# Kernel optimization log

Measured on AMD Instinct MI355X. Metric: run time of the kernel, lower is better.

## Reference

```python
import jax, jax.numpy as jnp
import numpy as np
import math

SEQ_LEN = 1024
NUM_FILTERS = 24
INPUT_DIM = 256
OUTPUT_DIM = 256
BATCH = 4


def _spectral_filters(seq_len, K):
    # Hankel matrix Z[i,j] = 2 / ((i+j)^3 - (i+j)), i,j in 1..L (use_hankel_L=False)
    entries = np.arange(1, seq_len + 1, dtype=np.float64)
    ipj = entries[:, None] + entries[None, :]
    Z = 2.0 / (ipj ** 3 - ipj)
    sigma, phi = np.linalg.eigh(Z)
    phi_k = phi[:, -K:] * (sigma[-K:] ** 0.25)
    return jnp.asarray(phi_k, dtype=jnp.float32)  # [L, K]


def setup_inputs() -> dict:
    key = jax.random.key(0)
    k1, k2, k3 = jax.random.split(key, 3)
    scale = (NUM_FILTERS * INPUT_DIM) ** (-0.5)
    x = jax.random.normal(k1, (BATCH, SEQ_LEN, INPUT_DIM), dtype=jnp.float32)
    phi = _spectral_filters(SEQ_LEN, NUM_FILTERS)
    M_phi_plus = jax.random.normal(k2, (NUM_FILTERS, INPUT_DIM, OUTPUT_DIM), dtype=jnp.float32) * scale
    M_phi_minus = jax.random.normal(k3, (NUM_FILTERS, INPUT_DIM, OUTPUT_DIM), dtype=jnp.float32) * scale
    return {"x": x, "phi": phi, "M_phi_plus": M_phi_plus, "M_phi_minus": M_phi_minus}


def reference(x, phi, M_phi_plus, M_phi_minus):
    B, L, I = x.shape
    n = 1 << math.ceil(math.log2(2 * L - 1))  # FFT length (2048 for L=1024)
    # alternating sign: +1 at even positions, -1 at odd (sgn[:,1::2] *= -1)
    sgn = jnp.where(jnp.arange(L) % 2 == 1, -1.0, 1.0).astype(jnp.float32)
    # FFT of filters: [F, K]
    V = jnp.fft.rfft(phi.astype(jnp.float32), n=n, axis=0)
    # FFT of input and sign-modulated input: [B, F, I]
    X = jnp.fft.rfft(x, n=n, axis=1)
    Xs = jnp.fft.rfft(x * sgn[None, :, None], n=n, axis=1)
    # pointwise multiply in frequency, broadcast over K: [B, F, K, I]
    U_plus = jnp.fft.irfft(V[None, :, :, None] * X[:, :, None, :], n=n, axis=1)[:, :L]
    U_minus = jnp.fft.irfft(V[None, :, :, None] * Xs[:, :, None, :], n=n, axis=1)[:, :L]
    U_minus = U_minus * sgn[None, :, None, None]
    # spectral projection: [B, L, O]
    out = jnp.einsum('blki,kio->blo', U_plus, M_phi_plus)
    out = out + jnp.einsum('blki,kio->blo', U_minus, M_phi_minus)
    return out
```

## Files before the change

### kernel.cpp

```cpp
#include <hip/hip_runtime.h>


#define ZB_ 12582912

typedef __attribute__((ext_vector_type(8))) short bf16x8;
typedef __attribute__((ext_vector_type(4))) float f32x4;

__device__ inline unsigned short f2bf(float f) {
    unsigned u = __float_as_uint(f);
    u += 0x7FFFu + ((u >> 16) & 1u);
    return (unsigned short)(u >> 16);
}

__device__ inline void gl16(const unsigned short* g, unsigned short* l) {
    __builtin_amdgcn_global_load_lds((const __attribute__((address_space(1))) void*)g,
                                     (__attribute__((address_space(3))) void*)l, 16, 0, 0);
}

__global__ __launch_bounds__(256) void k_prep_all(const float* __restrict__ x,
                                                  const float* __restrict__ phi,
                                                  const float* __restrict__ Mp,
                                                  const float* __restrict__ Mm,
                                                  unsigned short* __restrict__ xb,
                                                  unsigned short* __restrict__ ToepA,
                                                  unsigned short* __restrict__ MbT) {
    __shared__ float tile[32][33];
    int bid = blockIdx.x, tid = threadIdx.x;
    if (bid < 1024) {
        int i = (bid * 256 + tid) * 4;
        float4 v = *(const float4*)(x + i);
        ushort4 o;
        o.x = f2bf(v.x); o.y = f2bf(v.y); o.z = f2bf(v.z); o.w = f2bf(v.w);
        int row = i >> 8, col = i & 255;
        int dst = (row << 8) | (col & 192) | ((col & 63) ^ ((row & 7) << 3));
        *(ushort4*)(xb + dst) = o;
    } else if (bid < 1792) {
        int r = bid - 1024;
        int kk = r >> 4;
        int dm = (r & 15) - 1;
        int k = (kk < 24) ? kk : kk - 24;
        int i = tid >> 1, j0 = (tid & 1) * 32;
        unsigned short* dst = ToepA + ((size_t)kk * 16 + (dm + 1)) * 8192 + i * 64;
        int sw = (i & 7) << 3;
#pragma unroll
        for (int q = 0; q < 8; ++q) {
            int j = j0 + q * 4;
            unsigned short e[4];
#pragma unroll
            for (int ee = 0; ee < 4; ++ee) {
                int t = dm * 64 + i - (j + ee);
                float v = 0.f;
                if (t >= 0 && t < 1024) {
                    v = phi[t * 24 + k];
                    if (kk >= 24 && (t & 1)) v = -v;
                }
                e[ee] = f2bf(v);
            }
            ushort4 ov; ov.x = e[0]; ov.y = e[1]; ov.z = e[2]; ov.w = e[3];
            *(ushort4*)(dst + (j ^ sw)) = ov;
        }
    } else {
        int flat = bid - 1792;
        int kk = flat >> 6, rr = flat & 63;
        int i0 = (rr >> 3) * 32, o0 = (rr & 7) * 32;
        int tx = tid & 31, ty = tid >> 5;
        const float* src = ((kk < 24) ? Mp : Mm) + (size_t)((kk < 24) ? kk : kk - 24) * 65536;
        for (int j = 0; j < 4; ++j)
            tile[ty + j * 8][tx] = src[(i0 + ty + j * 8) * 256 + o0 + tx];
        __syncthreads();
        for (int j = 0; j < 4; ++j) {
            int orow = o0 + ty + j * 8, i = i0 + tx;
            int ic = (i & 192) | ((i & 63) ^ ((orow & 7) << 3));
            MbT[(size_t)kk * 65536 + orow * 256 + ic] = f2bf(tile[tx][ty + j * 8]);
        }
    }
}

__global__ __launch_bounds__(256, 2) void k_stage1(const unsigned short* __restrict__ xb0,
                                                   const unsigned short* __restrict__ MbT,
                                                   unsigned short* __restrict__ Z) {
    __shared__ unsigned short Ab[2][8192];
    __shared__ unsigned short Bb[3][8192];
    int tid = threadIdx.x, lane = tid & 63, w = tid >> 6;
    int wm = w >> 1, wn = w & 1;
    int m0 = blockIdx.x * 128;
    int kk = blockIdx.y >> 1;
    int o0 = (blockIdx.y & 1) * 128;
    int b  = blockIdx.z;
    const unsigned short* xb_b = xb0 + (size_t)b * 262144;
    unsigned short* Zb = Z + (size_t)b * ZB_;
    const unsigned short* Bsrc = MbT + (size_t)kk * 65536;
    int l16 = lane & 15, kofs = (lane >> 4) * 8;
    int sw = (l16 & 7) << 3;
    int r8 = lane >> 3, cg = lane & 7;

    int arow[4], brow[4], lofs[4];
#pragma unroll
    for (int q = 0; q < 4; ++q) {
        int rr = q * 32 + w * 8 + r8;
        arow[q] = (m0 + rr) * 256 + cg * 8;
        brow[q] = (o0 + rr) * 256 + cg * 8;
        lofs[q] = q * 2048 + w * 512;
    }

    f32x4 acc[4][4];
    for (int i = 0; i < 4; ++i)
        for (int j = 0; j < 4; ++j) {
            acc[i][j][0] = 0.f; acc[i][j][1] = 0.f; acc[i][j][2] = 0.f; acc[i][j][3] = 0.f;
        }

    auto stageA = [&](int bi, int ko) {
#pragma unroll
        for (int q = 0; q < 4; ++q) gl16(xb_b + arow[q] + ko * 64, &Ab[bi][0] + lofs[q]);
    };
    auto stageB = [&](int bi, int ko) {
#pragma unroll
        for (int q = 0; q < 4; ++q) gl16(Bsrc + brow[q] + ko * 64, &Bb[bi][0] + lofs[q]);
    };

    stageA(0, 0); stageB(0, 0); stageB(1, 1);

    for (int ko = 0; ko < 4; ++ko) {
        if (ko < 3) { asm volatile("s_waitcnt vmcnt(4)" ::: "memory"); }
        else        { asm volatile("s_waitcnt vmcnt(0)" ::: "memory"); }
        __builtin_amdgcn_sched_barrier(0);
        __builtin_amdgcn_s_barrier();
        __builtin_amdgcn_sched_barrier(0);
        if (ko < 3) stageA((ko + 1) & 1, ko + 1);
        if (ko < 2) stageB((ko + 2) % 3, ko + 2);

        const unsigned short* Abase = &Ab[ko & 1][0];
        const unsigned short* Bbase = &Bb[ko % 3][0];
        __builtin_amdgcn_s_setprio(1);
#pragma unroll
        for (int ks = 0; ks < 2; ++ks) {
            int koX = (ks * 32 + kofs) ^ sw;
            bf16x8 af[4], bfv[4];
#pragma unroll
            for (int mi = 0; mi < 4; ++mi)
                af[mi] = *(const bf16x8*)(Abase + (wm * 64 + mi * 16 + l16) * 64 + koX);
#pragma unroll
            for (int ni = 0; ni < 4; ++ni)
                bfv[ni] = *(const bf16x8*)(Bbase + (wn * 64 + ni * 16 + l16) * 64 + koX);
#pragma unroll
            for (int mi = 0; mi < 4; ++mi)
#pragma unroll
                for (int ni = 0; ni < 4; ++ni)
                    acc[mi][ni] = __builtin_amdgcn_mfma_f32_16x16x32_bf16(af[mi], bfv[ni], acc[mi][ni], 0, 0, 0);
        }
        __builtin_amdgcn_s_setprio(0);
    }

    int r4 = (lane >> 4) * 4;
    for (int mi = 0; mi < 4; ++mi) {
        int sbase = m0 + wm * 64 + mi * 16 + r4;
        for (int ni = 0; ni < 4; ++ni) {
            int o = o0 + wn * 64 + ni * 16 + l16;
            ushort4 pk;
            pk.x = f2bf(acc[mi][ni][0]); pk.y = f2bf(acc[mi][ni][1]);
            pk.z = f2bf(acc[mi][ni][2]); pk.w = f2bf(acc[mi][ni][3]);
            *(ushort4*)(Zb + (size_t)kk * 262144 + (size_t)o * 1024 + (sbase ^ ((o & 7) << 3))) = pk;
        }
    }
}

__global__ __launch_bounds__(256, 2) void k_stage2(const unsigned short* __restrict__ Z,
                                                   const unsigned short* __restrict__ ToepA,
                                                   float* __restrict__ partial, int kkpg) {
    __shared__ unsigned short Abuf[2][8192];
    __shared__ unsigned short Zbuf[3][8192];
    int tid = threadIdx.x, lane = tid & 63, w = tid >> 6;
    int wm = w >> 1, wn = w & 1;

    int gy = gridDim.y, nwg = 4 * gy * gridDim.z;
    int orig = blockIdx.x + blockIdx.y * 4 + blockIdx.z * 4 * gy;
    int wg = (orig & 7) * (nwg >> 3) + (orig >> 3);
    int pr = wg & 3;
    int yy = (wg >> 2) % gy;
    int zz = (wg >> 2) / gy;
    int o0 = (yy & 1) * 128;
    int b  = yy >> 1;
    int kgi = zz;
    int kk0 = kgi * kkpg;

    int l16 = lane & 15, kofs = (lane >> 4) * 8;
    int sw = (l16 & 7) << 3;
    int r8 = lane >> 3, cg = lane & 7;

    const unsigned short* Zb = Z + (size_t)b * ZB_;
    float* pb = partial + ((size_t)b * gridDim.z + kgi) * 262144;

    int arow[4], zrow[4], lofs[4];
#pragma unroll
    for (int q = 0; q < 4; ++q) {
        int rr = q * 32 + w * 8 + r8;
        arow[q] = rr * 64 + cg * 8;
        zrow[q] = (o0 + rr) * 1024 + cg * 8;
        lofs[q] = q * 2048 + w * 512;
    }

    for (int half = 0; half < 2; ++half) {
        int lb = half ? (7 - pr) : pr;
        int l0 = lb * 128;
        int nch = 2 * lb + 2;
        int total = kkpg * nch;

        f32x4 acc[4][4];
        for (int i = 0; i < 4; ++i)
            for (int j = 0; j < 4; ++j) {
                acc[i][j][0] = 0.f; acc[i][j][1] = 0.f; acc[i][j][2] = 0.f; acc[i][j][3] = 0.f;
            }

        __syncthreads();

        auto stageA = [&](int bi, int kka, int didx) {
            const unsigned short* gA = ToepA + ((size_t)kka * 16 + didx) * 8192;
#pragma unroll
            for (int q = 0; q < 4; ++q) gl16(gA + arow[q], &Abuf[bi][0] + lofs[q]);
        };
        auto stageZ = [&](int bi, int kka, int s0) {
            const unsigned short* gZ = Zb + (size_t)kka * 262144 + s0;
#pragma unroll
            for (int q = 0; q < 4; ++q) gl16(gZ + zrow[q], &Zbuf[bi][0] + lofs[q]);
        };
        auto compute = [&](int ba, int bz) {
            const unsigned short* Abase = &Abuf[ba][0];
            const unsigned short* Zbase = &Zbuf[bz][0];
            __builtin_amdgcn_s_setprio(1);
#pragma unroll
            for (int ks = 0; ks < 2; ++ks) {
                int koX = (ks * 32 + kofs) ^ sw;
                bf16x8 af[4], bfv[4];
#pragma unroll
                for (int mi = 0; mi < 4; ++mi)
                    af[mi] = *(const bf16x8*)(Abase + (wm * 64 + mi * 16 + l16) * 64 + koX);
#pragma unroll
                for (int ni = 0; ni < 4; ++ni)
                    bfv[ni] = *(const bf16x8*)(Zbase + (wn * 64 + ni * 16 + l16) * 64 + koX);
#pragma unroll
                for (int mi = 0; mi < 4; ++mi)
#pragma unroll
                    for (int ni = 0; ni < 4; ++ni)
                        acc[mi][ni] = __builtin_amdgcn_mfma_f32_16x16x32_bf16(af[mi], bfv[ni], acc[mi][ni], 0, 0, 0);
            }
            __builtin_amdgcn_s_setprio(0);
        };

        stageA(0, kk0, 2 * lb + 1);
        stageZ(0, kk0, 0);
        stageZ(1, kk0, 64);

        int scA = 1, kkA = 0;
        int scZ = 2, kkZ = 0;
        if (scZ == nch) { scZ = 0; kkZ = 1; }
        int jz = 2;

        for (int j = 0; j < total - 1; ++j) {
            asm volatile("s_waitcnt vmcnt(4)" ::: "memory");
            __builtin_amdgcn_sched_barrier(0);
            __builtin_amdgcn_s_barrier();
            __builtin_amdgcn_sched_barrier(0);
            stageA((j + 1) & 1, kk0 + kkA, 2 * lb - scA + 1);
            ++scA; if (scA == nch) { scA = 0; ++kkA; }
            if (jz < total) {
                stageZ(jz % 3, kk0 + kkZ, scZ * 64);
                ++scZ; if (scZ == nch) { scZ = 0; ++kkZ; }
                ++jz;
            }
            compute(j & 1, j % 3);
        }
        asm volatile("s_waitcnt vmcnt(0)" ::: "memory");
        __builtin_amdgcn_sched_barrier(0);
        __builtin_amdgcn_s_barrier();
        __builtin_amdgcn_sched_barrier(0);
        compute((total - 1) & 1, (total - 1) % 3);

        int r4 = (lane >> 4) * 4;
        for (int mi = 0; mi < 4; ++mi) {
            int l = l0 + wm * 64 + mi * 16 + r4;
            for (int ni = 0; ni < 4; ++ni) {
                int o = o0 + wn * 64 + ni * 16 + l16;
                float* dst = pb + (size_t)l * 256 + o;
                dst[0]   = acc[mi][ni][0];
                dst[256] = acc[mi][ni][1];
                dst[512] = acc[mi][ni][2];
                dst[768] = acc[mi][ni][3];
            }
        }
    }
}

__global__ void k_reduce(const float* __restrict__ partial, float* __restrict__ outg, int kg) {
    const float* pb = partial + (size_t)blockIdx.y * kg * 262144;
    int i = (blockIdx.x * 256 + threadIdx.x) * 4;
    float4 s = *(const float4*)(pb + i);
    for (int kgi = 1; kgi < kg; ++kgi) {
        float4 v = *(const float4*)(pb + (size_t)kgi * 262144 + i);
        s.x += v.x; s.y += v.y; s.z += v.z; s.w += v.w;
    }
    *(float4*)(outg + (size_t)blockIdx.y * 262144 + i) = s;
}

extern "C" void kernel_launch(void* const* d_in, const int* in_sizes, int n_in,
                              void* d_out, int out_size, void* d_ws, size_t ws_size,
                              hipStream_t stream) {
    const float* x   = (const float*)d_in[0];
    const float* phi = (const float*)d_in[1];
    const float* Mp  = (const float*)d_in[2];
    const float* Mm  = (const float*)d_in[3];
    float* out = (float*)d_out;

    char* ws = (char*)d_ws;
    unsigned short* xb    = (unsigned short*)(ws);
    unsigned short* MbT   = (unsigned short*)(ws + 2097152);
    unsigned short* ToepA = (unsigned short*)(ws + 8388608);
    unsigned short* Zbuf  = (unsigned short*)(ws + 20971520);
    const size_t fixed = 20971520;

    int g = 4, kg = 16;
    auto need = [&](int gg, int kk) {
        return fixed + (size_t)gg * 25165824 + (size_t)gg * (size_t)kk * 1048576;
    };
    if (need(4, 16) > ws_size) {
        kg = 12;
        if (need(4, 12) > ws_size) {
            g = 2; kg = 16;
            if (need(2, 16) > ws_size) {
                kg = 12;
                if (need(2, 12) > ws_size) {
                    g = 1; kg = 16;
                    if (need(1, 16) > ws_size) {
                        kg = 12;
                        if (need(1, 12) > ws_size) kg = 6;
                    }
                }
            }
        }
    }
    float* partial = (float*)(ws + fixed + (size_t)g * 25165824);

    k_prep_all<<<dim3(4864), dim3(256), 0, stream>>>(x, phi, Mp, Mm, xb, ToepA, MbT);

    for (int b0 = 0; b0 < 4; b0 += g) {
        k_stage1<<<dim3(8, 96, g), dim3(256), 0, stream>>>(xb + (size_t)b0 * 262144, MbT, Zbuf);
        k_stage2<<<dim3(4, 2 * g, kg), dim3(256), 0, stream>>>(Zbuf, ToepA, partial, 48 / kg);
        k_reduce<<<dim3(256, g), dim3(256), 0, stream>>>(partial, out + (size_t)b0 * 262144, kg);
    }
}
```

Before: 147.7 us.

## Load Toeplitz A fragments directly to registers and quad-buffer Z in LDS

Stage2 stops staging the Toeplitz filter tile through LDS. Each wave now loads its A fragments straight from global memory into double-buffered registers, and Toeplitz storage is made unswizzled to match. Z gets a 4-deep LDS ring with a two-step unrolled pipeline and retuned vmcnt waits. This removes the A LDS traffic and its bank-conflict swizzle, but it costs more VGPRs, uncoalesced-ish 16B global loads per lane, and fragile hand-counted waitcnt values.

```diff
diff --git a/kernel.cpp b/kernel.cpp
--- a/kernel.cpp
+++ b/kernel.cpp
@@ -41,7 +41,6 @@
         int k = (kk < 24) ? kk : kk - 24;
         int i = tid >> 1, j0 = (tid & 1) * 32;
         unsigned short* dst = ToepA + ((size_t)kk * 16 + (dm + 1)) * 8192 + i * 64;
-        int sw = (i & 7) << 3;
 #pragma unroll
         for (int q = 0; q < 8; ++q) {
             int j = j0 + q * 4;
@@ -57,7 +56,7 @@
                 e[ee] = f2bf(v);
             }
             ushort4 ov; ov.x = e[0]; ov.y = e[1]; ov.z = e[2]; ov.w = e[3];
-            *(ushort4*)(dst + (j ^ sw)) = ov;
+            *(ushort4*)(dst + j) = ov;
         }
     } else {
         int flat = bid - 1792;
@@ -167,8 +166,7 @@
 __global__ __launch_bounds__(256, 2) void k_stage2(const unsigned short* __restrict__ Z,
                                                    const unsigned short* __restrict__ ToepA,
                                                    float* __restrict__ partial, int kkpg) {
-    __shared__ unsigned short Abuf[2][8192];
-    __shared__ unsigned short Zbuf[3][8192];
+    __shared__ unsigned short Zl[4][8192];
     int tid = threadIdx.x, lane = tid & 63, w = tid >> 6;
     int wm = w >> 1, wn = w & 1;
 
@@ -190,14 +188,19 @@
     const unsigned short* Zb = Z + (size_t)b * ZB_;
     float* pb = partial + ((size_t)b * gridDim.z + kgi) * 262144;
 
-    int arow[4], zrow[4], lofs[4];
+    int zrow[4], lofs[4];
 #pragma unroll
     for (int q = 0; q < 4; ++q) {
         int rr = q * 32 + w * 8 + r8;
-        arow[q] = rr * 64 + cg * 8;
         zrow[q] = (o0 + rr) * 1024 + cg * 8;
         lofs[q] = q * 2048 + w * 512;
     }
+    int aofs[4][2];
+#pragma unroll
+    for (int mi = 0; mi < 4; ++mi)
+#pragma unroll
+        for (int ks = 0; ks < 2; ++ks)
+            aofs[mi][ks] = (wm * 64 + mi * 16 + l16) * 64 + ks * 32 + kofs;
 
     for (int half = 0; half < 2; ++half) {
         int lb = half ? (7 - pr) : pr;
@@ -213,27 +216,26 @@
 
         __syncthreads();
 
-        auto stageA = [&](int bi, int kka, int didx) {
-            const unsigned short* gA = ToepA + ((size_t)kka * 16 + didx) * 8192;
-#pragma unroll
-            for (int q = 0; q < 4; ++q) gl16(gA + arow[q], &Abuf[bi][0] + lofs[q]);
+        auto zstage = [&](int bufi, int kkx, int sc) {
+            const unsigned short* gZ = Zb + (size_t)(kk0 + kkx) * 262144 + sc * 64;
+#pragma unroll
+            for (int q = 0; q < 4; ++q) gl16(gZ + zrow[q], &Zl[bufi][0] + lofs[q]);
         };
-        auto stageZ = [&](int bi, int kka, int s0) {
-            const unsigned short* gZ = Zb + (size_t)kka * 262144 + s0;
-#pragma unroll
-            for (int q = 0; q < 4; ++q) gl16(gZ + zrow[q], &Zbuf[bi][0] + lofs[q]);
+        auto aload = [&](bf16x8 (&dst)[4][2], int kkx, int sc) {
+            const unsigned short* gA = ToepA + ((size_t)(kk0 + kkx) * 16 + (2 * lb - sc + 1)) * 8192;
+#pragma unroll
+            for (int mi = 0; mi < 4; ++mi)
+#pragma unroll
+                for (int ks = 0; ks < 2; ++ks)
+                    dst[mi][ks] = *(const bf16x8*)(gA + aofs[mi][ks]);
         };
-        auto compute = [&](int ba, int bz) {
-            const unsigned short* Abase = &Abuf[ba][0];
-            const unsigned short* Zbase = &Zbuf[bz][0];
+        auto compute = [&](bf16x8 (&afr)[4][2], int bufi) {
+            const unsigned short* Zbase = &Zl[bufi][0];
             __builtin_amdgcn_s_setprio(1);
 #pragma unroll
             for (int ks = 0; ks < 2; ++ks) {
                 int koX = (ks * 32 + kofs) ^ sw;
-                bf16x8 af[4], bfv[4];
-#pragma unroll
-                for (int mi = 0; mi < 4; ++mi)
-                    af[mi] = *(const bf16x8*)(Abase + (wm * 64 + mi * 16 + l16) * 64 + koX);
+                bf16x8 bfv[4];
 #pragma unroll
                 for (int ni = 0; ni < 4; ++ni)
                     bfv[ni] = *(const bf16x8*)(Zbase + (wn * 64 + ni * 16 + l16) * 64 + koX);
@@ -241,39 +243,55 @@
                 for (int mi = 0; mi < 4; ++mi)
 #pragma unroll
                     for (int ni = 0; ni < 4; ++ni)
-                        acc[mi][ni] = __builtin_amdgcn_mfma_f32_16x16x32_bf16(af[mi], bfv[ni], acc[mi][ni], 0, 0, 0);
+                        acc[mi][ni] = __builtin_amdgcn_mfma_f32_16x16x32_bf16(afr[mi][ks], bfv[ni], acc[mi][ni], 0, 0, 0);
             }
             __builtin_amdgcn_s_setprio(0);
         };
 
-        stageA(0, kk0, 2 * lb + 1);
-        stageZ(0, kk0, 0);
-        stageZ(1, kk0, 64);
+        bf16x8 aR[4][2], aS[4][2];
+
+        zstage(0, 0, 0);
+        aload(aR, 0, 0);
+        zstage(1, 0, 1);
 
         int scA = 1, kkA = 0;
         int scZ = 2, kkZ = 0;
         if (scZ == nch) { scZ = 0; kkZ = 1; }
-        int jz = 2;
-
-        for (int j = 0; j < total - 1; ++j) {
-            asm volatile("s_waitcnt vmcnt(4)" ::: "memory");
+
+        for (int j = 0; j < total - 2; j += 2) {
+            aload(aS, kkA, scA);
+            ++scA; if (scA == nch) { scA = 0; ++kkA; }
+            zstage((j + 2) & 3, kkZ, scZ);
+            ++scZ; if (scZ == nch) { scZ = 0; ++kkZ; }
+            asm volatile("s_waitcnt vmcnt(24)" ::: "memory");
             __builtin_amdgcn_sched_barrier(0);
             __builtin_amdgcn_s_barrier();
             __builtin_amdgcn_sched_barrier(0);
-            stageA((j + 1) & 1, kk0 + kkA, 2 * lb - scA + 1);
+            compute(aR, j & 3);
+
+            aload(aR, kkA, scA);
             ++scA; if (scA == nch) { scA = 0; ++kkA; }
-            if (jz < total) {
-                stageZ(jz % 3, kk0 + kkZ, scZ * 64);
-                ++scZ; if (scZ == nch) { scZ = 0; ++kkZ; }
-                ++jz;
-            }
-            compute(j & 1, j % 3);
-        }
-        asm volatile("s_waitcnt vmcnt(0)" ::: "memory");
+            zstage((j + 3) & 3, kkZ, scZ);
+            ++scZ; if (scZ == nch) { scZ = 0; ++kkZ; }
+            asm volatile("s_waitcnt vmcnt(24)" ::: "memory");
+            __builtin_amdgcn_sched_barrier(0);
+            __builtin_amdgcn_s_barrier();
+            __builtin_amdgcn_sched_barrier(0);
+            compute(aS, (j + 1) & 3);
+        }
+
+        aload(aS, kkA, scA);
+        asm volatile("s_waitcnt vmcnt(20)" ::: "memory");
         __builtin_amdgcn_sched_barrier(0);
         __builtin_amdgcn_s_barrier();
         __builtin_amdgcn_sched_barrier(0);
-        compute((total - 1) & 1, (total - 1) % 3);
+        compute(aR, (total - 2) & 3);
+
+        asm volatile("s_waitcnt vmcnt(8)" ::: "memory");
+        __builtin_amdgcn_sched_barrier(0);
+        __builtin_amdgcn_s_barrier();
+        __builtin_amdgcn_sched_barrier(0);
+        compute(aS, (total - 1) & 3);
 
         int r4 = (lane >> 4) * 4;
         for (int mi = 0; mi < 4; ++mi) {
```

After: 199.2 us. +34.9%, slower.
